# Performance work log

Hardware: AMD Instinct MI355X
Metric: run time of the kernel (lower is better)

The kernel has to match this reference:

```python
import jax, jax.numpy as jnp
import numpy as np

N_NODES = 50000
N_EDGES = 600000
D = 128          # in_channels == hidden_channels
N_GRAPHS = 500
OUT = 10
N_LAYERS = 4


def setup_inputs() -> dict:
    key = jax.random.key(0)
    ks = jax.random.split(key, 9)
    s = 0.05
    x = jax.random.normal(ks[0], (N_NODES, D), dtype=jnp.float32)
    edge_index = jax.random.randint(ks[1], (2, N_EDGES), 0, N_NODES, dtype=jnp.int64)
    batch = jnp.sort(jax.random.randint(ks[2], (N_NODES,), 0, N_GRAPHS, dtype=jnp.int64))
    # GINConv MLP params, stacked over the 4 conv layers: Linear(D,D) -> ReLU -> Linear(D,D)
    W1 = jax.random.normal(ks[3], (N_LAYERS, D, D), dtype=jnp.float32) * s
    b1 = jax.random.normal(ks[4], (N_LAYERS, D), dtype=jnp.float32) * s
    W2 = jax.random.normal(ks[5], (N_LAYERS, D, D), dtype=jnp.float32) * s
    b2 = jax.random.normal(ks[6], (N_LAYERS, D), dtype=jnp.float32) * s
    lin_w = jax.random.normal(ks[7], (D, OUT), dtype=jnp.float32) * s
    lin_b = jax.random.normal(ks[8], (OUT,), dtype=jnp.float32) * s
    return {"x": x, "edge_index": edge_index, "batch": batch,
            "W1": W1, "b1": b1, "W2": W2, "b2": b2,
            "lin_w": lin_w, "lin_b": lin_b}


def reference(x, edge_index, batch, W1, b1, W2, b2, lin_w, lin_b):
    src, dst = edge_index[0], edge_index[1]
    h = x
    for i in range(N_LAYERS):
        # GINConv (eps=0): h_i <- MLP(h_i + sum_{j in N(i)} h_j)
        agg = jax.ops.segment_sum(h[src], dst, num_segments=N_NODES)  # [N, D]
        z = h + agg
        z = jnp.maximum(z @ W1[i] + b1[i], 0.0)
        h = z @ W2[i] + b2[i]
        if i < N_LAYERS - 1:  # relu after conv1..conv3, not conv4
            h = jnp.maximum(h, 0.0)
    hG = jax.ops.segment_sum(h, batch, num_segments=N_GRAPHS)  # global_add_pool [G, D]
    # dropout p=0.5 is identity in eval mode
    logits = hG @ lin_w + lin_b  # [G, OUT]
    return (hG, jax.nn.log_softmax(logits, axis=1))
```

## Files before the change

kernel.cpp:

```cpp
#include <hip/hip_runtime.h>
#include <hip/hip_bf16.h>

#define D 128

typedef __attribute__((ext_vector_type(8))) short bf8;
typedef __attribute__((ext_vector_type(4))) float f4;

__device__ inline unsigned short f2bf(float f){
  unsigned u = __float_as_uint(f);
  unsigned r = (u + 0x7fff + ((u >> 16) & 1)) >> 16;
  return (unsigned short)r;
}
__device__ inline float bflo(unsigned u){ return __uint_as_float(u << 16); }
__device__ inline float bfhi(unsigned u){ return __uint_as_float(u & 0xffff0000u); }


__global__ __launch_bounds__(256) void k_count(const int* __restrict__ dst, int* __restrict__ counts, int E){
  int e = blockIdx.x * 256 + threadIdx.x;
  if (e < E) atomicAdd(&counts[dst[e]], 1);
}

__global__ __launch_bounds__(256) void k_blocksum(const int* __restrict__ counts, int* __restrict__ partial, int N){
  __shared__ int sm[256];
  int i = blockIdx.x * 256 + threadIdx.x;
  int v = (i < N) ? counts[i] : 0;
  sm[threadIdx.x] = v; __syncthreads();
  for (int off = 128; off; off >>= 1){
    if (threadIdx.x < off) sm[threadIdx.x] += sm[threadIdx.x + off];
    __syncthreads();
  }
  if (threadIdx.x == 0) partial[blockIdx.x] = sm[0];
}

__global__ __launch_bounds__(256) void k_scanpartial(const int* __restrict__ partial, int* __restrict__ poff, int nb,
                                                     int* __restrict__ row_start, int N){
  __shared__ int sm[256];
  int t = threadIdx.x;
  int v = (t < nb) ? partial[t] : 0;
  sm[t] = v; __syncthreads();
  for (int off = 1; off < 256; off <<= 1){
    int x = (t >= off) ? sm[t - off] : 0;
    __syncthreads();
    sm[t] += x;
    __syncthreads();
  }
  if (t < nb) poff[t] = sm[t] - v;
  if (t == 0) row_start[N] = sm[255];
}

__global__ __launch_bounds__(256) void k_blockscan(const int* __restrict__ counts, const int* __restrict__ poff,
                                                   int* __restrict__ row_start, int N){
  __shared__ int sm[256];
  int i = blockIdx.x * 256 + threadIdx.x;
  int v = (i < N) ? counts[i] : 0;
  sm[threadIdx.x] = v; __syncthreads();
  for (int off = 1; off < 256; off <<= 1){
    int t = (threadIdx.x >= off) ? sm[threadIdx.x - off] : 0;
    __syncthreads();
    sm[threadIdx.x] += t;
    __syncthreads();
  }
  if (i < N) row_start[i] = poff[blockIdx.x] + sm[threadIdx.x] - v;
}

__global__ __launch_bounds__(256) void k_fill(const int* __restrict__ src, const int* __restrict__ dst,
                                              const int* __restrict__ row_start, int* __restrict__ fillcnt,
                                              int* __restrict__ srcs, int E){
  int e = blockIdx.x * 256 + threadIdx.x;
  if (e < E){
    int d = dst[e];
    int pos = row_start[d] + atomicAdd(&fillcnt[d], 1);
    srcs[pos] = src[e];
  }
}


__global__ __launch_bounds__(256) void k_cast(const float* __restrict__ in, unsigned short* __restrict__ outb, int n8){
  int i = blockIdx.x * 256 + threadIdx.x;
  if (i >= n8) return;
  const float4* p = (const float4*)(in + (size_t)i * 8);
  float4 a = p[0], b = p[1];
  union { unsigned short s[8]; uint4 u; } o;
  o.s[0]=f2bf(a.x); o.s[1]=f2bf(a.y); o.s[2]=f2bf(a.z); o.s[3]=f2bf(a.w);
  o.s[4]=f2bf(b.x); o.s[5]=f2bf(b.y); o.s[6]=f2bf(b.z); o.s[7]=f2bf(b.w);
  *(uint4*)(outb + (size_t)i * 8) = o.u;
}

__global__ __launch_bounds__(256) void k_packWT(const float* __restrict__ W1, const float* __restrict__ W2,
                                                unsigned short* __restrict__ WT){
  int idx = blockIdx.x * 256 + threadIdx.x;
  int m = idx >> 14;
  int r = idx & 16383;
  int n = r >> 7, k = r & 127;
  const float* W = (m < 4) ? (W1 + (size_t)m * D * D) : (W2 + (size_t)(m - 4) * D * D);
  WT[idx] = f2bf(W[(size_t)k * D + n]);
}


__global__ __launch_bounds__(256) void k_agg(const unsigned short* __restrict__ hb, const int* __restrict__ row_start,
                                             const int* __restrict__ srcs, unsigned short* __restrict__ zb, int N){
  int wid  = (blockIdx.x * 256 + threadIdx.x) >> 6;
  int lane = threadIdx.x & 63;
  if (wid >= N) return;
  int g  = lane >> 4;
  int sl = lane & 15;
  const uint4* h4 = (const uint4*)hb;

  float a0=0,a1=0,a2=0,a3=0,a4=0,a5=0,a6=0,a7=0;
  if (g == 0){
    uint4 v = h4[(size_t)wid * 16 + sl];
    a0 += bflo(v.x); a1 += bfhi(v.x); a2 += bflo(v.y); a3 += bfhi(v.y);
    a4 += bflo(v.z); a5 += bfhi(v.z); a6 += bflo(v.w); a7 += bfhi(v.w);
  }
  int beg = row_start[wid], end = row_start[wid + 1];
  int e = beg + g;
  for (; e + 4 < end; e += 8){
    int s0 = srcs[e], s1 = srcs[e + 4];
    uint4 v0 = h4[(size_t)s0 * 16 + sl];
    uint4 v1 = h4[(size_t)s1 * 16 + sl];
    a0 += bflo(v0.x) + bflo(v1.x); a1 += bfhi(v0.x) + bfhi(v1.x);
    a2 += bflo(v0.y) + bflo(v1.y); a3 += bfhi(v0.y) + bfhi(v1.y);
    a4 += bflo(v0.z) + bflo(v1.z); a5 += bfhi(v0.z) + bfhi(v1.z);
    a6 += bflo(v0.w) + bflo(v1.w); a7 += bfhi(v0.w) + bfhi(v1.w);
  }
  if (e < end){
    uint4 v = h4[(size_t)srcs[e] * 16 + sl];
    a0 += bflo(v.x); a1 += bfhi(v.x); a2 += bflo(v.y); a3 += bfhi(v.y);
    a4 += bflo(v.z); a5 += bfhi(v.z); a6 += bflo(v.w); a7 += bfhi(v.w);
  }
  a0 += __shfl_xor(a0, 16); a1 += __shfl_xor(a1, 16);
  a2 += __shfl_xor(a2, 16); a3 += __shfl_xor(a3, 16);
  a4 += __shfl_xor(a4, 16); a5 += __shfl_xor(a5, 16);
  a6 += __shfl_xor(a6, 16); a7 += __shfl_xor(a7, 16);
  a0 += __shfl_xor(a0, 32); a1 += __shfl_xor(a1, 32);
  a2 += __shfl_xor(a2, 32); a3 += __shfl_xor(a3, 32);
  a4 += __shfl_xor(a4, 32); a5 += __shfl_xor(a5, 32);
  a6 += __shfl_xor(a6, 32); a7 += __shfl_xor(a7, 32);
  if (g == 0){
    uint4 o;
    o.x = ((unsigned)f2bf(a1) << 16) | (unsigned)f2bf(a0);
    o.y = ((unsigned)f2bf(a3) << 16) | (unsigned)f2bf(a2);
    o.z = ((unsigned)f2bf(a5) << 16) | (unsigned)f2bf(a4);
    o.w = ((unsigned)f2bf(a7) << 16) | (unsigned)f2bf(a6);
    ((uint4*)zb)[(size_t)wid * 16 + sl] = o;
  }
}


template<int LAST>
__global__ __launch_bounds__(256) void k_mlp(const unsigned short* __restrict__ A,
                                             const unsigned short* __restrict__ WT1,
                                             const float* __restrict__ b1,
                                             const unsigned short* __restrict__ WT2,
                                             const float* __restrict__ b2,
                                             unsigned short* __restrict__ out, int M){
  __shared__ unsigned short Wl[128 * 136];
  __shared__ unsigned short Al[64 * 136];
  int tid = threadIdx.x;
  int row0 = blockIdx.x * 64;
  int w = tid >> 6, lane = tid & 63;
  int lr = lane & 15, lk = (lane >> 4) * 8;
  int rr = tid >> 4, cc = (tid & 15) * 8;

  #pragma unroll
  for (int it = 0; it < 8; ++it){
    int r = it * 16 + rr;
    *(uint4*)&Wl[r * 136 + cc] = *(const uint4*)&WT1[(size_t)r * D + cc];
  }
  #pragma unroll
  for (int it = 0; it < 4; ++it){
    int r = it * 16 + rr;
    int row = row0 + r;
    uint4 v = make_uint4(0, 0, 0, 0);
    if (row < M) v = *(const uint4*)&A[(size_t)row * D + cc];
    *(uint4*)&Al[r * 136 + cc] = v;
  }
  __syncthreads();

  f4 acc[8];
  bf8 af[4];
  #pragma unroll
  for (int i = 0; i < 8; ++i) acc[i] = (f4)(0.f);
  #pragma unroll
  for (int ks = 0; ks < 4; ++ks) af[ks] = *(const bf8*)&Al[(w * 16 + lr) * 136 + ks * 32 + lk];
  #pragma unroll
  for (int nt = 0; nt < 8; ++nt)
    #pragma unroll
    for (int ks = 0; ks < 4; ++ks){
      bf8 b = *(const bf8*)&Wl[(nt * 16 + lr) * 136 + ks * 32 + lk];
      acc[nt] = __builtin_amdgcn_mfma_f32_16x16x32_bf16(af[ks], b, acc[nt], 0, 0, 0);
    }
  {
    int rbase = w * 16 + (lane >> 4) * 4;
    #pragma unroll
    for (int nt = 0; nt < 8; ++nt){
      int col = nt * 16 + lr;
      float bb = b1[col];
      #pragma unroll
      for (int j = 0; j < 4; ++j)
        Al[(rbase + j) * 136 + col] = f2bf(fmaxf(acc[nt][j] + bb, 0.f));
    }
  }
  __syncthreads();
  #pragma unroll
  for (int it = 0; it < 8; ++it){
    int r = it * 16 + rr;
    *(uint4*)&Wl[r * 136 + cc] = *(const uint4*)&WT2[(size_t)r * D + cc];
  }
  __syncthreads();
  #pragma unroll
  for (int i = 0; i < 8; ++i) acc[i] = (f4)(0.f);
  #pragma unroll
  for (int ks = 0; ks < 4; ++ks) af[ks] = *(const bf8*)&Al[(w * 16 + lr) * 136 + ks * 32 + lk];
  #pragma unroll
  for (int nt = 0; nt < 8; ++nt)
    #pragma unroll
    for (int ks = 0; ks < 4; ++ks){
      bf8 b = *(const bf8*)&Wl[(nt * 16 + lr) * 136 + ks * 32 + lk];
      acc[nt] = __builtin_amdgcn_mfma_f32_16x16x32_bf16(af[ks], b, acc[nt], 0, 0, 0);
    }
  {
    int rbase = row0 + w * 16 + (lane >> 4) * 4;
    #pragma unroll
    for (int nt = 0; nt < 8; ++nt){
      int col = nt * 16 + lr;
      float bb = b2[col];
      #pragma unroll
      for (int j = 0; j < 4; ++j){
        int row = rbase + j;
        if (row < M){
          float v = acc[nt][j] + bb;
          if (!LAST) v = fmaxf(v, 0.f);
          out[(size_t)row * D + col] = f2bf(v);
        }
      }
    }
  }
}


__global__ __launch_bounds__(256) void k_pool(const unsigned short* __restrict__ hb, const int* __restrict__ batch,
                                              float* __restrict__ hG, int N){
  int g = blockIdx.x * 256 + threadIdx.x;
  int chunk = g >> 5;
  int dg = g & 31;
  int n0 = chunk * 16;
  if (n0 >= N) return;
  int n1 = n0 + 16; if (n1 > N) n1 = N;
  float ax = 0.f, ay = 0.f, az = 0.f, aw = 0.f;
  int cur = batch[n0];
  for (int n = n0; n < n1; ++n){
    int b = batch[n];
    uint2 v = *(const uint2*)&hb[(size_t)n * D + dg * 4];
    if (b != cur){
      float* p = &hG[(size_t)cur * D + dg * 4];
      atomicAdd(p + 0, ax); atomicAdd(p + 1, ay); atomicAdd(p + 2, az); atomicAdd(p + 3, aw);
      ax = ay = az = aw = 0.f; cur = b;
    }
    ax += bflo(v.x); ay += bfhi(v.x); az += bflo(v.y); aw += bfhi(v.y);
  }
  float* p = &hG[(size_t)cur * D + dg * 4];
  atomicAdd(p + 0, ax); atomicAdd(p + 1, ay); atomicAdd(p + 2, az); atomicAdd(p + 3, aw);
}


__global__ __launch_bounds__(64) void k_head(const float* __restrict__ hG, const float* __restrict__ lw,
                                             const float* __restrict__ lb, float* __restrict__ out){
  int gph = blockIdx.x;
  int lane = threadIdx.x;
  float logit = -INFINITY;
  if (lane < 10){
    float s = lb[lane];
    const float* hg = &hG[(size_t)gph * D];
    #pragma unroll 8
    for (int k = 0; k < D; ++k) s += hg[k] * lw[k * 10 + lane];
    logit = s;
  }
  float m = logit;
  for (int off = 32; off; off >>= 1) m = fmaxf(m, __shfl_down(m, off));
  m = __shfl(m, 0);
  float e = (lane < 10) ? expf(logit - m) : 0.f;
  float ssum = e;
  for (int off = 32; off; off >>= 1) ssum += __shfl_down(ssum, off);
  ssum = __shfl(ssum, 0);
  if (lane < 10) out[(size_t)gph * 10 + lane] = logit - m - logf(ssum);
}


extern "C" void kernel_launch(void* const* d_in, const int* in_sizes, int n_in,
                              void* d_out, int out_size, void* d_ws, size_t ws_size,
                              hipStream_t stream){
  const float* x  = (const float*)d_in[0];
  const int*   ei = (const int*)d_in[1];
  const int*   batch = (const int*)d_in[2];
  const float* W1 = (const float*)d_in[3];
  const float* b1 = (const float*)d_in[4];
  const float* W2 = (const float*)d_in[5];
  const float* b2 = (const float*)d_in[6];
  const float* lw = (const float*)d_in[7];
  const float* lb = (const float*)d_in[8];
  float* out = (float*)d_out;

  int N = in_sizes[0] / D;
  int E = in_sizes[1] / 2;
  int G = out_size / (D + 10);
  const int* src = ei;
  const int* dst = ei + E;

  char* w = (char*)d_ws;
  size_t off = 0;
  auto alloc = [&](size_t bytes) -> char* {
    char* p = w + off;
    off = (off + bytes + 255) & ~(size_t)255;
    return p;
  };
  unsigned short* h_bf  = (unsigned short*)alloc((size_t)N * D * 2);
  unsigned short* z_bf  = (unsigned short*)alloc((size_t)N * D * 2);
  unsigned short* WT    = (unsigned short*)alloc((size_t)8 * D * D * 2);
  int nb = (N + 255) / 256;
  int* row_start = (int*)alloc((size_t)(N + 1) * 4);
  int* counts    = (int*)alloc((size_t)N * 4);
  int* fillcnt   = (int*)alloc((size_t)N * 4);
  int* partial   = (int*)alloc((size_t)nb * 4);
  int* poff      = (int*)alloc((size_t)nb * 4);
  int* srcs      = (int*)alloc((size_t)E * 4);

  hipMemsetAsync(counts,  0, (size_t)N * 4, stream);
  hipMemsetAsync(fillcnt, 0, (size_t)N * 4, stream);
  hipMemsetAsync(d_out,   0, (size_t)out_size * 4, stream);

  int n8 = N * D / 8;
  k_cast<<<(n8 + 255) / 256, 256, 0, stream>>>(x, h_bf, n8);
  k_packWT<<<512, 256, 0, stream>>>(W1, W2, WT);

  int ge = (E + 255) / 256;
  k_count<<<ge, 256, 0, stream>>>(dst, counts, E);
  k_blocksum<<<nb, 256, 0, stream>>>(counts, partial, N);
  k_scanpartial<<<1, 256, 0, stream>>>(partial, poff, nb, row_start, N);
  k_blockscan<<<nb, 256, 0, stream>>>(counts, poff, row_start, N);
  k_fill<<<ge, 256, 0, stream>>>(src, dst, row_start, fillcnt, srcs, E);

  int gagg = (N + 3) / 4;
  int gm = (N + 63) / 64;
  for (int i = 0; i < 4; ++i){
    k_agg<<<gagg, 256, 0, stream>>>(h_bf, row_start, srcs, z_bf, N);
    if (i < 3)
      k_mlp<0><<<gm, 256, 0, stream>>>(z_bf, WT + (size_t)i * D * D, b1 + (size_t)i * D,
                                       WT + (size_t)(4 + i) * D * D, b2 + (size_t)i * D, h_bf, N);
    else
      k_mlp<1><<<gm, 256, 0, stream>>>(z_bf, WT + (size_t)i * D * D, b1 + (size_t)i * D,
                                       WT + (size_t)(4 + i) * D * D, b2 + (size_t)i * D, h_bf, N);
  }

  int gp = (((N + 15) / 16) * 32 + 255) / 256;
  k_pool<<<gp, 256, 0, stream>>>(h_bf, batch, out, N);
  k_head<<<G, 64, 0, stream>>>(out, lw, lb, out + (size_t)G * D);
}
```

Before: 391.9 us.

## Fuse neighbor aggregation into MLP kernel with ping-pong hidden buffers

Merges the separate gather-aggregate kernel into the per-layer MLP kernel. Each wave aggregates its 16 rows straight into shared memory, so the intermediate z buffer no longer makes a round trip through global memory. Weights are now read directly from global memory (via cache) instead of being staged in LDS. The fill kernel reuses the counts array through atomicSub, which removes one memset and one buffer, and hidden states alternate between two buffers. The risks are less parallelism in the gather phase, since each wave walks 16 nodes in sequence, and uncached weight fragment loads in the MFMA loop.

```diff
diff --git a/kernel.cpp b/kernel.cpp
--- a/kernel.cpp
+++ b/kernel.cpp
@@ -64,13 +64,13 @@
 }
 
 __global__ __launch_bounds__(256) void k_fill(const int* __restrict__ src, const int* __restrict__ dst,
-                                              const int* __restrict__ row_start, int* __restrict__ fillcnt,
+                                              const int* __restrict__ row_start, int* __restrict__ counts,
                                               int* __restrict__ srcs, int E){
   int e = blockIdx.x * 256 + threadIdx.x;
   if (e < E){
     int d = dst[e];
-    int pos = row_start[d] + atomicAdd(&fillcnt[d], 1);
-    srcs[pos] = src[e];
+    int v = atomicSub(&counts[d], 1);
+    srcs[row_start[d] + v - 1] = src[e];
   }
 }
 
@@ -97,88 +97,70 @@
 }
 
 
-__global__ __launch_bounds__(256) void k_agg(const unsigned short* __restrict__ hb, const int* __restrict__ row_start,
-                                             const int* __restrict__ srcs, unsigned short* __restrict__ zb, int N){
-  int wid  = (blockIdx.x * 256 + threadIdx.x) >> 6;
-  int lane = threadIdx.x & 63;
-  if (wid >= N) return;
-  int g  = lane >> 4;
-  int sl = lane & 15;
-  const uint4* h4 = (const uint4*)hb;
-
-  float a0=0,a1=0,a2=0,a3=0,a4=0,a5=0,a6=0,a7=0;
-  if (g == 0){
-    uint4 v = h4[(size_t)wid * 16 + sl];
-    a0 += bflo(v.x); a1 += bfhi(v.x); a2 += bflo(v.y); a3 += bfhi(v.y);
-    a4 += bflo(v.z); a5 += bfhi(v.z); a6 += bflo(v.w); a7 += bfhi(v.w);
-  }
-  int beg = row_start[wid], end = row_start[wid + 1];
-  int e = beg + g;
-  for (; e + 4 < end; e += 8){
-    int s0 = srcs[e], s1 = srcs[e + 4];
-    uint4 v0 = h4[(size_t)s0 * 16 + sl];
-    uint4 v1 = h4[(size_t)s1 * 16 + sl];
-    a0 += bflo(v0.x) + bflo(v1.x); a1 += bfhi(v0.x) + bfhi(v1.x);
-    a2 += bflo(v0.y) + bflo(v1.y); a3 += bfhi(v0.y) + bfhi(v1.y);
-    a4 += bflo(v0.z) + bflo(v1.z); a5 += bfhi(v0.z) + bfhi(v1.z);
-    a6 += bflo(v0.w) + bflo(v1.w); a7 += bfhi(v0.w) + bfhi(v1.w);
-  }
-  if (e < end){
-    uint4 v = h4[(size_t)srcs[e] * 16 + sl];
-    a0 += bflo(v.x); a1 += bfhi(v.x); a2 += bflo(v.y); a3 += bfhi(v.y);
-    a4 += bflo(v.z); a5 += bfhi(v.z); a6 += bflo(v.w); a7 += bfhi(v.w);
-  }
-  a0 += __shfl_xor(a0, 16); a1 += __shfl_xor(a1, 16);
-  a2 += __shfl_xor(a2, 16); a3 += __shfl_xor(a3, 16);
-  a4 += __shfl_xor(a4, 16); a5 += __shfl_xor(a5, 16);
-  a6 += __shfl_xor(a6, 16); a7 += __shfl_xor(a7, 16);
-  a0 += __shfl_xor(a0, 32); a1 += __shfl_xor(a1, 32);
-  a2 += __shfl_xor(a2, 32); a3 += __shfl_xor(a3, 32);
-  a4 += __shfl_xor(a4, 32); a5 += __shfl_xor(a5, 32);
-  a6 += __shfl_xor(a6, 32); a7 += __shfl_xor(a7, 32);
-  if (g == 0){
-    uint4 o;
-    o.x = ((unsigned)f2bf(a1) << 16) | (unsigned)f2bf(a0);
-    o.y = ((unsigned)f2bf(a3) << 16) | (unsigned)f2bf(a2);
-    o.z = ((unsigned)f2bf(a5) << 16) | (unsigned)f2bf(a4);
-    o.w = ((unsigned)f2bf(a7) << 16) | (unsigned)f2bf(a6);
-    ((uint4*)zb)[(size_t)wid * 16 + sl] = o;
-  }
-}
-
-
 template<int LAST>
-__global__ __launch_bounds__(256) void k_mlp(const unsigned short* __restrict__ A,
-                                             const unsigned short* __restrict__ WT1,
-                                             const float* __restrict__ b1,
-                                             const unsigned short* __restrict__ WT2,
-                                             const float* __restrict__ b2,
-                                             unsigned short* __restrict__ out, int M){
-  __shared__ unsigned short Wl[128 * 136];
+__global__ __launch_bounds__(256) void k_layer(const unsigned short* __restrict__ h,
+                                               const int* __restrict__ row_start,
+                                               const int* __restrict__ srcs,
+                                               const unsigned short* __restrict__ WT1,
+                                               const float* __restrict__ b1,
+                                               const unsigned short* __restrict__ WT2,
+                                               const float* __restrict__ b2,
+                                               unsigned short* __restrict__ out, int M){
   __shared__ unsigned short Al[64 * 136];
   int tid = threadIdx.x;
   int row0 = blockIdx.x * 64;
   int w = tid >> 6, lane = tid & 63;
+  int g = lane >> 4, sl = lane & 15;
+  const uint4* h4 = (const uint4*)h;
+
+  for (int i = 0; i < 16; ++i){
+    int node = row0 + w * 16 + i;
+    float a0=0,a1=0,a2=0,a3=0,a4=0,a5=0,a6=0,a7=0;
+    if (node < M){
+      if (g == 0){
+        uint4 v = h4[(size_t)node * 16 + sl];
+        a0 += bflo(v.x); a1 += bfhi(v.x); a2 += bflo(v.y); a3 += bfhi(v.y);
+        a4 += bflo(v.z); a5 += bfhi(v.z); a6 += bflo(v.w); a7 += bfhi(v.w);
+      }
+      int beg = row_start[node], end = row_start[node + 1];
+      int e = beg + g;
+      for (; e + 4 < end; e += 8){
+        int s0 = srcs[e], s1 = srcs[e + 4];
+        uint4 v0 = h4[(size_t)s0 * 16 + sl];
+        uint4 v1 = h4[(size_t)s1 * 16 + sl];
+        a0 += bflo(v0.x) + bflo(v1.x); a1 += bfhi(v0.x) + bfhi(v1.x);
+        a2 += bflo(v0.y) + bflo(v1.y); a3 += bfhi(v0.y) + bfhi(v1.y);
+        a4 += bflo(v0.z) + bflo(v1.z); a5 += bfhi(v0.z) + bfhi(v1.z);
+        a6 += bflo(v0.w) + bflo(v1.w); a7 += bfhi(v0.w) + bfhi(v1.w);
+      }
+      if (e < end){
+        uint4 v = h4[(size_t)srcs[e] * 16 + sl];
+        a0 += bflo(v.x); a1 += bfhi(v.x); a2 += bflo(v.y); a3 += bfhi(v.y);
+        a4 += bflo(v.z); a5 += bfhi(v.z); a6 += bflo(v.w); a7 += bfhi(v.w);
+      }
+    }
+    a0 += __shfl_xor(a0, 16); a1 += __shfl_xor(a1, 16);
+    a2 += __shfl_xor(a2, 16); a3 += __shfl_xor(a3, 16);
+    a4 += __shfl_xor(a4, 16); a5 += __shfl_xor(a5, 16);
+    a6 += __shfl_xor(a6, 16); a7 += __shfl_xor(a7, 16);
+    a0 += __shfl_xor(a0, 32); a1 += __shfl_xor(a1, 32);
+    a2 += __shfl_xor(a2, 32); a3 += __shfl_xor(a3, 32);
+    a4 += __shfl_xor(a4, 32); a5 += __shfl_xor(a5, 32);
+    a6 += __shfl_xor(a6, 32); a7 += __shfl_xor(a7, 32);
+    if (g == 0){
+      uint4 o;
+      o.x = ((unsigned)f2bf(a1) << 16) | (unsigned)f2bf(a0);
+      o.y = ((unsigned)f2bf(a3) << 16) | (unsigned)f2bf(a2);
+      o.z = ((unsigned)f2bf(a5) << 16) | (unsigned)f2bf(a4);
+      o.w = ((unsigned)f2bf(a7) << 16) | (unsigned)f2bf(a6);
+      *(uint4*)&Al[(w * 16 + i) * 136 + sl * 8] = o;
+    }
+  }
+
   int lr = lane & 15, lk = (lane >> 4) * 8;
-  int rr = tid >> 4, cc = (tid & 15) * 8;
-
-  #pragma unroll
-  for (int it = 0; it < 8; ++it){
-    int r = it * 16 + rr;
-    *(uint4*)&Wl[r * 136 + cc] = *(const uint4*)&WT1[(size_t)r * D + cc];
-  }
-  #pragma unroll
-  for (int it = 0; it < 4; ++it){
-    int r = it * 16 + rr;
-    int row = row0 + r;
-    uint4 v = make_uint4(0, 0, 0, 0);
-    if (row < M) v = *(const uint4*)&A[(size_t)row * D + cc];
-    *(uint4*)&Al[r * 136 + cc] = v;
-  }
-  __syncthreads();
-
   f4 acc[8];
   bf8 af[4];
+
   #pragma unroll
   for (int i = 0; i < 8; ++i) acc[i] = (f4)(0.f);
   #pragma unroll
@@ -187,7 +169,7 @@
   for (int nt = 0; nt < 8; ++nt)
     #pragma unroll
     for (int ks = 0; ks < 4; ++ks){
-      bf8 b = *(const bf8*)&Wl[(nt * 16 + lr) * 136 + ks * 32 + lk];
+      bf8 b = *(const bf8*)&WT1[(size_t)(nt * 16 + lr) * D + ks * 32 + lk];
       acc[nt] = __builtin_amdgcn_mfma_f32_16x16x32_bf16(af[ks], b, acc[nt], 0, 0, 0);
     }
   {
@@ -201,13 +183,6 @@
         Al[(rbase + j) * 136 + col] = f2bf(fmaxf(acc[nt][j] + bb, 0.f));
     }
   }
-  __syncthreads();
-  #pragma unroll
-  for (int it = 0; it < 8; ++it){
-    int r = it * 16 + rr;
-    *(uint4*)&Wl[r * 136 + cc] = *(const uint4*)&WT2[(size_t)r * D + cc];
-  }
-  __syncthreads();
   #pragma unroll
   for (int i = 0; i < 8; ++i) acc[i] = (f4)(0.f);
   #pragma unroll
@@ -216,7 +191,7 @@
   for (int nt = 0; nt < 8; ++nt)
     #pragma unroll
     for (int ks = 0; ks < 4; ++ks){
-      bf8 b = *(const bf8*)&Wl[(nt * 16 + lr) * 136 + ks * 32 + lk];
+      bf8 b = *(const bf8*)&WT2[(size_t)(nt * 16 + lr) * D + ks * 32 + lk];
       acc[nt] = __builtin_amdgcn_mfma_f32_16x16x32_bf16(af[ks], b, acc[nt], 0, 0, 0);
     }
   {
@@ -315,19 +290,17 @@
     return p;
   };
   unsigned short* h_bf  = (unsigned short*)alloc((size_t)N * D * 2);
-  unsigned short* z_bf  = (unsigned short*)alloc((size_t)N * D * 2);
+  unsigned short* h2_bf = (unsigned short*)alloc((size_t)N * D * 2);
   unsigned short* WT    = (unsigned short*)alloc((size_t)8 * D * D * 2);
   int nb = (N + 255) / 256;
   int* row_start = (int*)alloc((size_t)(N + 1) * 4);
   int* counts    = (int*)alloc((size_t)N * 4);
-  int* fillcnt   = (int*)alloc((size_t)N * 4);
   int* partial   = (int*)alloc((size_t)nb * 4);
   int* poff      = (int*)alloc((size_t)nb * 4);
   int* srcs      = (int*)alloc((size_t)E * 4);
 
-  hipMemsetAsync(counts,  0, (size_t)N * 4, stream);
-  hipMemsetAsync(fillcnt, 0, (size_t)N * 4, stream);
-  hipMemsetAsync(d_out,   0, (size_t)out_size * 4, stream);
+  hipMemsetAsync(counts, 0, (size_t)N * 4, stream);
+  hipMemsetAsync(d_out,  0, (size_t)out_size * 4, stream);
 
   int n8 = N * D / 8;
   k_cast<<<(n8 + 255) / 256, 256, 0, stream>>>(x, h_bf, n8);
@@ -338,21 +311,24 @@
   k_blocksum<<<nb, 256, 0, stream>>>(counts, partial, N);
   k_scanpartial<<<1, 256, 0, stream>>>(partial, poff, nb, row_start, N);
   k_blockscan<<<nb, 256, 0, stream>>>(counts, poff, row_start, N);
-  k_fill<<<ge, 256, 0, stream>>>(src, dst, row_start, fillcnt, srcs, E);
-
-  int gagg = (N + 3) / 4;
+  k_fill<<<ge, 256, 0, stream>>>(src, dst, row_start, counts, srcs, E);
+
   int gm = (N + 63) / 64;
+  unsigned short* hin  = h_bf;
+  unsigned short* hout = h2_bf;
   for (int i = 0; i < 4; ++i){
-    k_agg<<<gagg, 256, 0, stream>>>(h_bf, row_start, srcs, z_bf, N);
     if (i < 3)
-      k_mlp<0><<<gm, 256, 0, stream>>>(z_bf, WT + (size_t)i * D * D, b1 + (size_t)i * D,
-                                       WT + (size_t)(4 + i) * D * D, b2 + (size_t)i * D, h_bf, N);
+      k_layer<0><<<gm, 256, 0, stream>>>(hin, row_start, srcs,
+                                         WT + (size_t)i * D * D, b1 + (size_t)i * D,
+                                         WT + (size_t)(4 + i) * D * D, b2 + (size_t)i * D, hout, N);
     else
-      k_mlp<1><<<gm, 256, 0, stream>>>(z_bf, WT + (size_t)i * D * D, b1 + (size_t)i * D,
-                                       WT + (size_t)(4 + i) * D * D, b2 + (size_t)i * D, h_bf, N);
+      k_layer<1><<<gm, 256, 0, stream>>>(hin, row_start, srcs,
+                                         WT + (size_t)i * D * D, b1 + (size_t)i * D,
+                                         WT + (size_t)(4 + i) * D * D, b2 + (size_t)i * D, hout, N);
+    unsigned short* t = hin; hin = hout; hout = t;
   }
 
   int gp = (((N + 15) / 16) * 32 + 255) / 256;
-  k_pool<<<gp, 256, 0, stream>>>(h_bf, batch, out, N);
+  k_pool<<<gp, 256, 0, stream>>>(hin, batch, out, N);
   k_head<<<G, 64, 0, stream>>>(out, lw, lb, out + (size_t)G * D);
 }
```

Result: slower. 469.7 us (+19.8%).
